# Performance work log

Measured on AMD Instinct MI355X. Metric: run time of the kernel, lower is better.

The kernel has to match this reference:

```python
import jax, jax.numpy as jnp
import numpy as np

B, N, C = 8, 4096, 1024
H, D = 16, 64
FF = 4096
EPS_ATTN = 1e-6
EPS_LN = 1e-5


def layer_norm(x, g, b, eps=EPS_LN):
    mu = jnp.mean(x, axis=-1, keepdims=True)
    var = jnp.mean(jnp.square(x - mu), axis=-1, keepdims=True)
    return (x - mu) * jax.lax.rsqrt(var + eps) * g + b


def phi(x):
    # elu(x) + 1
    return jnp.where(x > 0, x + 1.0, jnp.exp(x))


def setup_inputs() -> dict:
    key = jax.random.key(0)
    ks = jax.random.split(key, 8)
    src = jax.random.normal(ks[0], (B, N, C), dtype=jnp.float32)
    lengths = jax.random.randint(ks[1], (B,), int(0.75 * N), N + 1)
    src_key_padding_mask = jnp.arange(N)[None, :] >= lengths[:, None]
    s = 0.02
    qkv_w = jax.random.normal(ks[2], (3 * C, C), dtype=jnp.float32) * s
    qkv_b = jnp.zeros((3 * C,), jnp.float32)
    out_w = jax.random.normal(ks[3], (C, C), dtype=jnp.float32) * s
    out_b = jnp.zeros((C,), jnp.float32)
    w1 = jax.random.normal(ks[4], (FF, C), dtype=jnp.float32) * s
    b1 = jnp.zeros((FF,), jnp.float32)
    w2 = jax.random.normal(ks[5], (C, FF), dtype=jnp.float32) * s
    b2 = jnp.zeros((C,), jnp.float32)
    ln1_g = jnp.ones((C,), jnp.float32)
    ln1_b = jnp.zeros((C,), jnp.float32)
    ln2_g = jnp.ones((C,), jnp.float32)
    ln2_b = jnp.zeros((C,), jnp.float32)
    return dict(src=src, src_key_padding_mask=src_key_padding_mask,
                qkv_w=qkv_w, qkv_b=qkv_b, out_w=out_w, out_b=out_b,
                w1=w1, b1=b1, w2=w2, b2=b2,
                ln1_g=ln1_g, ln1_b=ln1_b, ln2_g=ln2_g, ln2_b=ln2_b)


def linear_attention(x, mask, qkv_w, qkv_b, out_w, out_b):
    b, n, c = x.shape
    qkv = (x @ qkv_w.T + qkv_b).reshape(b, n, 3, H, D)
    qkv = jnp.transpose(qkv, (2, 0, 3, 1, 4))  # [3,B,H,N,D]
    q, k, v = qkv[0], qkv[1], qkv[2]
    qf, kf = phi(q), phi(k)
    valid = (~mask).astype(kf.dtype)[:, None, :, None]  # [B,1,N,1]
    kf = kf * valid
    v = v * valid
    kv = jnp.einsum('bhnd,bhne->bhde', kf, v)          # [B,H,D,D]
    z = kf.sum(axis=2)                                  # [B,H,D]
    y_num = jnp.einsum('bhnd,bhde->bhne', qf, kv)       # [B,H,N,D]
    y_den = jnp.maximum(jnp.einsum('bhnd,bhd->bhn', qf, z), EPS_ATTN)
    y = y_num / y_den[..., None]
    y = jnp.transpose(y, (0, 2, 1, 3)).reshape(b, n, c)
    return y @ out_w.T + out_b


def reference(src, src_key_padding_mask, qkv_w, qkv_b, out_w, out_b,
              w1, b1, w2, b2, ln1_g, ln1_b, ln2_g, ln2_b):
    # pre-norm: attention block
    attn_out = linear_attention(layer_norm(src, ln1_g, ln1_b), src_key_padding_mask,
                                qkv_w, qkv_b, out_w, out_b)
    x = src + attn_out
    # pre-norm: FFN block (exact gelu, matching torch F.gelu default)
    h = jax.nn.gelu(layer_norm(x, ln2_g, ln2_b) @ w1.T + b1, approximate=False)
    return x + (h @ w2.T + b2)
```

## Files before the change

### kernel.cpp

```cpp
#include <hip/hip_runtime.h>
#include <cmath>
#include <cstdint>

#define MTOK 32768
#define CDIM 1024
#define SEQ  4096
#define NHEAD 16
#define HDIM 64
#define FFDIM 4096

typedef __attribute__((ext_vector_type(8))) short short8;
typedef __attribute__((ext_vector_type(4))) float f32x4;

static __device__ __forceinline__ float b2f(unsigned short u){
  union { unsigned int i; float f; } c; c.i = ((unsigned int)u)<<16; return c.f;
}
static __device__ __forceinline__ unsigned short f2b(float f){
  union { float f; unsigned int i; } c; c.f = f;
  return (unsigned short)((c.i + 0x7fffu + ((c.i>>16)&1u)) >> 16);
}
static __device__ __forceinline__ void async16(const void* g, void* l){
  __builtin_amdgcn_global_load_lds((const __attribute__((address_space(1))) void*)g,
                                   (__attribute__((address_space(3))) void*)l, 16, 0, 0);
}

__global__ void detect_mask_kernel(const unsigned int* __restrict__ m, int* __restrict__ flag){
  __shared__ int any;
  if(threadIdx.x==0) any=0;
  __syncthreads();
  int loc=0;
  for(int i=threadIdx.x;i<8192;i+=256) if(m[i]>1u) loc=1;
  if(loc) atomicOr(&any,1);
  __syncthreads();
  if(threadIdx.x==0) *flag=any;
}
__global__ void decode_mask_kernel(const void* __restrict__ m, const int* __restrict__ flag,
                                   float* __restrict__ validf){
  int i = blockIdx.x*256 + threadIdx.x;
  int pad = (*flag) ? (int)((const unsigned char*)m)[i] : ((const int*)m)[i];
  validf[i] = pad ? 0.f : 1.f;
}

__global__ void cast_bf16_kernel(const float* __restrict__ x, unsigned short* __restrict__ y, int n){
  int i = (blockIdx.x*256 + threadIdx.x)*4;
  if(i>=n) return;
  float4 v = *(const float4*)(x+i);
  ushort4 o; o.x=f2b(v.x); o.y=f2b(v.y); o.z=f2b(v.z); o.w=f2b(v.w);
  *(ushort4*)(y+i)=o;
}

__global__ __launch_bounds__(256) void ln_kernel(const float* __restrict__ x,
    const float* __restrict__ g, const float* __restrict__ bt, unsigned short* __restrict__ out){
  int row = blockIdx.x, t = threadIdx.x;
  const float* xr = x + (size_t)row*CDIM;
  float4 v = *(const float4*)(xr + t*4);
  float s1 = v.x+v.y+v.z+v.w;
  float s2 = v.x*v.x+v.y*v.y+v.z*v.z+v.w*v.w;
  #pragma unroll
  for(int off=32; off>0; off>>=1){ s1+=__shfl_down(s1,off); s2+=__shfl_down(s2,off); }
  __shared__ float a1[4], a2[4];
  __shared__ float mu_s, rs_s;
  if((t&63)==0){ a1[t>>6]=s1; a2[t>>6]=s2; }
  __syncthreads();
  if(t==0){
    float u1=a1[0]+a1[1]+a1[2]+a1[3], u2=a2[0]+a2[1]+a2[2]+a2[3];
    float mu=u1*(1.f/CDIM);
    mu_s=mu; rs_s=rsqrtf(u2*(1.f/CDIM)-mu*mu+1e-5f);
  }
  __syncthreads();
  float mu=mu_s, rs=rs_s;
  float4 gg=*(const float4*)(g+t*4), bb=*(const float4*)(bt+t*4);
  ushort4 o;
  o.x=f2b((v.x-mu)*rs*gg.x+bb.x);
  o.y=f2b((v.y-mu)*rs*gg.y+bb.y);
  o.z=f2b((v.z-mu)*rs*gg.z+bb.z);
  o.w=f2b((v.w-mu)*rs*gg.w+bb.w);
  *(ushort4*)(out+(size_t)row*CDIM+t*4)=o;
}

template<int MODE>
__global__ __launch_bounds__(256,2) void gemm_bt(
    const unsigned short* __restrict__ A, const unsigned short* __restrict__ Bw,
    const float* __restrict__ bias, const float* __restrict__ extra,
    float* __restrict__ Cf, unsigned short* __restrict__ Cb,
    int M, int N, int K)
{
  __shared__ __align__(16) unsigned short As[128*64];
  __shared__ __align__(16) unsigned short Bs[128*64];
  const int tid = threadIdx.x;
  const int wave = tid>>6, lane = tid&63;
  const int wm = wave>>1, wn = wave&1;
  const int f   = blockIdx.y * gridDim.x + blockIdx.x;
  const int xcd = f & 7, kk = f >> 3;
  const int nx  = kk % gridDim.x;
  const int ny  = (kk / gridDim.x) * 8 + xcd;
  const int m0 = ny*128, n0 = nx*128;
  const int lrow = lane>>3;
  const int gcol = (((lane&7) ^ lrow))*8;

  f32x4 acc[4][4];
  #pragma unroll
  for(int i=0;i<4;i++)
    #pragma unroll
    for(int j=0;j<4;j++) acc[i][j]=(f32x4)(0.f);

  const int ar = wm*64 + (lane&15);
  const int br = wn*64 + (lane&15);
  const int kc = lane>>4;
  const int xorv = lane&7;

  for(int kt=0; kt<K; kt+=64){
    #pragma unroll
    for(int it=0; it<4; it++){
      int wo = wave*4+it;
      int r  = wo*8 + lrow;
      async16(A  + (size_t)(m0+r)*K + kt + gcol, (void*)&As[wo*512]);
      async16(Bw + (size_t)(n0+r)*K + kt + gcol, (void*)&Bs[wo*512]);
    }
    __syncthreads();
    #pragma unroll
    for(int ks=0; ks<2; ks++){
      const int ch = ((ks*4 + kc) ^ xorv)*8;
      short8 a[4], b[4];
      #pragma unroll
      for(int i=0;i<4;i++){
        a[i]=*(const short8*)&As[(ar+i*16)*64 + ch];
        b[i]=*(const short8*)&Bs[(br+i*16)*64 + ch];
      }
      #pragma unroll
      for(int i=0;i<4;i++)
        #pragma unroll
        for(int j=0;j<4;j++)
          acc[i][j]=__builtin_amdgcn_mfma_f32_16x16x32_bf16(a[i],b[j],acc[i][j],0,0,0);
    }
    __syncthreads();
  }
  const int rbase = m0 + wm*64 + (lane>>4)*4;
  const int cbase = n0 + wn*64 + (lane&15);
  #pragma unroll
  for(int mi=0;mi<4;mi++){
    #pragma unroll
    for(int i=0;i<4;i++){
      int m = rbase + mi*16 + i;
      #pragma unroll
      for(int ni=0;ni<4;ni++){
        int n = cbase + ni*16;
        float v = acc[mi][ni][i] + bias[n];
        if(MODE==0){
          float valid = extra[m];
          int part = n>>10;
          float p = (v>0.f)? (v+1.f) : __expf(v);
          float r = (part==0)? p : (part==1? p*valid : v*valid);
          Cb[(size_t)m*N + n] = f2b(r);
        } else if(MODE==1){
          size_t off=(size_t)m*N+n;
          Cf[off] = v + extra[off];
        } else if(MODE==2){
          float gl = 0.5f*v*(1.f+erff(v*0.70710678118654752f));
          Cb[(size_t)m*N+n] = f2b(gl);
        } else {
          size_t off=(size_t)m*N+n;
          Cf[off] += v;
        }
      }
    }
  }
}

__global__ __launch_bounds__(256) void kvz_partial_kernel(
    const unsigned short* __restrict__ qkv, float* __restrict__ kvp, float* __restrict__ zp)
{
  const int chunk = blockIdx.x;
  const int bh = blockIdx.y;
  const int b = bh>>4, h = bh&15;
  const int t = threadIdx.x;
  __shared__ float kfs[16][64];
  __shared__ float vs[16][64];
  float acc[4][4]={{0}}; float zacc[4]={0};
  const int td=t&15, te=t>>4;
  const int d0=td*4, e0=te*4;
  const int lr=t>>4, lc=(t&15)*4;
  for(int s=0;s<16;s++){
    size_t m  = (size_t)(b*SEQ + chunk*256 + s*16 + lr);
    size_t rb = m*3072 + (size_t)h*64;
    ushort4 k4 = *(const ushort4*)(qkv + rb + 1024 + lc);
    ushort4 v4 = *(const ushort4*)(qkv + rb + 2048 + lc);
    __syncthreads();
    kfs[lr][lc]=b2f(k4.x); kfs[lr][lc+1]=b2f(k4.y); kfs[lr][lc+2]=b2f(k4.z); kfs[lr][lc+3]=b2f(k4.w);
    vs [lr][lc]=b2f(v4.x); vs [lr][lc+1]=b2f(v4.y); vs [lr][lc+2]=b2f(v4.z); vs [lr][lc+3]=b2f(v4.w);
    __syncthreads();
    #pragma unroll
    for(int n=0;n<16;n++){
      float4 kq=*(const float4*)&kfs[n][d0];
      float4 vv=*(const float4*)&vs[n][e0];
      float kqa[4]={kq.x,kq.y,kq.z,kq.w};
      float vva[4]={vv.x,vv.y,vv.z,vv.w};
      #pragma unroll
      for(int i=0;i<4;i++)
        #pragma unroll
        for(int j=0;j<4;j++) acc[i][j]+=kqa[i]*vva[j];
      if(te==0){ zacc[0]+=kq.x; zacc[1]+=kq.y; zacc[2]+=kq.z; zacc[3]+=kq.w; }
    }
  }
  const int pidx = bh*16 + chunk;
  float* kvd = kvp + (size_t)pidx*4096;
  #pragma unroll
  for(int i=0;i<4;i++){
    float4 o={acc[i][0],acc[i][1],acc[i][2],acc[i][3]};
    *(float4*)(kvd + (d0+i)*64 + e0)=o;
  }
  if(te==0){
    float4 o={zacc[0],zacc[1],zacc[2],zacc[3]};
    *(float4*)(zp + (size_t)pidx*64 + d0)=o;
  }
}

__global__ void kvz_reduce_kernel(const float* __restrict__ kvp, const float* __restrict__ zp,
                                  float* __restrict__ kv, float* __restrict__ z){
  int bh = blockIdx.x, t = threadIdx.x;
  for(int j=t; j<4096; j+=256){
    float s=0;
    for(int c=0;c<16;c++) s += kvp[((size_t)bh*16+c)*4096 + j];
    kv[(size_t)bh*4096 + j] = s;
  }
  if(t<64){
    float s=0;
    for(int c=0;c<16;c++) s += zp[((size_t)bh*16+c)*64 + t];
    z[bh*64+t]=s;
  }
}

__global__ __launch_bounds__(256) void y_kernel(
    const unsigned short* __restrict__ qkv, const float* __restrict__ kv,
    const float* __restrict__ z, unsigned short* __restrict__ ybuf)
{
  const int nch = blockIdx.x;
  const int bh  = blockIdx.y;
  const int b = bh>>4, h = bh&15;
  const int t = threadIdx.x;
  __shared__ float kvs[64][64];
  __shared__ float qfs[64][68];
  __shared__ float zs[64];
  for(int j=t*4; j<4096; j+=1024){
    float4 vv=*(const float4*)(kv+(size_t)bh*4096+j);
    ((float*)kvs)[j]=vv.x; ((float*)kvs)[j+1]=vv.y; ((float*)kvs)[j+2]=vv.z; ((float*)kvs)[j+3]=vv.w;
  }
  if(t<64) zs[t]=z[bh*64+t];
  for(int s=0;s<4;s++){
    int row=s*16+(t>>4), col=(t&15)*4;
    size_t m=(size_t)(b*SEQ+nch*64+row);
    ushort4 q4=*(const ushort4*)(qkv+m*3072+(size_t)h*64+col);
    qfs[row][col]=b2f(q4.x); qfs[row][col+1]=b2f(q4.y); qfs[row][col+2]=b2f(q4.z); qfs[row][col+3]=b2f(q4.w);
  }
  __syncthreads();
  const int tn=t>>4, te=t&15;
  const int nr0=tn*4, e0=te*4;
  float acc[4][4]={{0}}; float den[4]={0};
  #pragma unroll 4
  for(int d=0;d<64;d++){
    float4 kv4=*(const float4*)&kvs[d][e0];
    float zd=zs[d];
    #pragma unroll
    for(int i=0;i<4;i++){
      float q=qfs[nr0+i][d];
      acc[i][0]+=q*kv4.x; acc[i][1]+=q*kv4.y; acc[i][2]+=q*kv4.z; acc[i][3]+=q*kv4.w;
      den[i]+=q*zd;
    }
  }
  #pragma unroll
  for(int i=0;i<4;i++){
    float inv=1.f/fmaxf(den[i],1e-6f);
    ushort4 o;
    o.x=f2b(acc[i][0]*inv); o.y=f2b(acc[i][1]*inv); o.z=f2b(acc[i][2]*inv); o.w=f2b(acc[i][3]*inv);
    size_t m=(size_t)(b*SEQ+nch*64+nr0+i);
    *(ushort4*)(ybuf+m*1024+(size_t)h*64+e0)=o;
  }
}

extern "C" void kernel_launch(void* const* d_in, const int* in_sizes, int n_in,
                              void* d_out, int out_size, void* d_ws, size_t ws_size,
                              hipStream_t stream)
{
  const float* src   = (const float*)d_in[0];
  const void*  mask  = d_in[1];
  const float* qkv_w = (const float*)d_in[2];
  const float* qkv_b = (const float*)d_in[3];
  const float* out_w = (const float*)d_in[4];
  const float* out_b = (const float*)d_in[5];
  const float* w1    = (const float*)d_in[6];
  const float* b1    = (const float*)d_in[7];
  const float* w2    = (const float*)d_in[8];
  const float* b2    = (const float*)d_in[9];
  const float* ln1g  = (const float*)d_in[10];
  const float* ln1b  = (const float*)d_in[11];
  const float* ln2g  = (const float*)d_in[12];
  const float* ln2b  = (const float*)d_in[13];
  float* out = (float*)d_out;
  char* ws = (char*)d_ws;

  size_t o = 0;
  int* flag = (int*)(ws);                         o += 256;
  float* validf = (float*)(ws+o);                 o += (size_t)MTOK*4;
  unsigned short* wqb = (unsigned short*)(ws+o);  o += (size_t)3072*1024*2;
  unsigned short* wob = (unsigned short*)(ws+o);  o += (size_t)1024*1024*2;
  unsigned short* w1b = (unsigned short*)(ws+o);  o += (size_t)4096*1024*2;
  unsigned short* w2b = (unsigned short*)(ws+o);  o += (size_t)1024*4096*2;
  unsigned short* bufA = (unsigned short*)(ws+o); o += (size_t)MTOK*1024*2;
  char* R = ws+o;                                 o += (size_t)MTOK*4096*2;
  unsigned short* qkvbuf = (unsigned short*)R;
  float* kvp = (float*)(R + (size_t)MTOK*3072*2);
  float* zp  = (float*)(R + (size_t)MTOK*3072*2 + (size_t)2048*4096*4);
  unsigned short* hbuf = (unsigned short*)R;
  float* kv = (float*)(ws+o);                     o += (size_t)128*4096*4;
  float* zv = (float*)(ws+o);                     o += (size_t)128*64*4;

  detect_mask_kernel<<<1,256,0,stream>>>((const unsigned int*)mask, flag);
  decode_mask_kernel<<<MTOK/256,256,0,stream>>>(mask, flag, validf);
  cast_bf16_kernel<<<3072,256,0,stream>>>(qkv_w, wqb, 3072*1024);
  cast_bf16_kernel<<<1024,256,0,stream>>>(out_w, wob, 1024*1024);
  cast_bf16_kernel<<<4096,256,0,stream>>>(w1,  w1b, 4096*1024);
  cast_bf16_kernel<<<8192,256,0,stream>>>(w2,  w2b, 1024*4096);

  ln_kernel<<<MTOK,256,0,stream>>>(src, ln1g, ln1b, bufA);
  gemm_bt<0><<<dim3(3072/128, MTOK/128),256,0,stream>>>(bufA, wqb, qkv_b, validf, nullptr, qkvbuf, MTOK,3072,1024);
  kvz_partial_kernel<<<dim3(16,128),256,0,stream>>>(qkvbuf, kvp, zp);
  kvz_reduce_kernel<<<128,256,0,stream>>>(kvp, zp, kv, zv);
  y_kernel<<<dim3(64,128),256,0,stream>>>(qkvbuf, kv, zv, bufA);
  gemm_bt<1><<<dim3(1024/128, MTOK/128),256,0,stream>>>(bufA, wob, out_b, src, out, nullptr, MTOK,1024,1024);
  ln_kernel<<<MTOK,256,0,stream>>>(out, ln2g, ln2b, bufA);
  gemm_bt<2><<<dim3(4096/128, MTOK/128),256,0,stream>>>(bufA, w1b, b1, nullptr, nullptr, hbuf, MTOK,4096,1024);
  gemm_bt<3><<<dim3(1024/128, MTOK/128),256,0,stream>>>(hbuf, w2b, b2, nullptr, out, nullptr, MTOK,1024,4096);
}
```

Before: 1.471 ms.

## Rewrite GEMM as 256x256 tile, 8-wave, double-buffered pipelined kernel

The bf16 GEMM moves from 128x128 tiles with 4 waves and a single LDS buffer to 256x256 tiles with 8 waves and double-buffered LDS. Global-to-LDS async loads for the next K-step are issued between four quadrant MFMA phases, with explicit vmcnt/lgkmcnt waits, barriers and s_setprio raising priority around the MFMA bursts. The aim is to overlap memory traffic with matrix math and raise arithmetic intensity per tile. In exchange it uses more LDS and registers per block, launches fewer blocks (the out-projection and FFN2 GEMMs get only 512 blocks), and its correctness rests on hand-tuned wait counts.

```diff
diff --git a/kernel.cpp b/kernel.cpp
--- a/kernel.cpp
+++ b/kernel.cpp
@@ -79,88 +79,148 @@
 }
 
 template<int MODE>
-__global__ __launch_bounds__(256,2) void gemm_bt(
+__global__ __launch_bounds__(512,2) void gemm_bt(
     const unsigned short* __restrict__ A, const unsigned short* __restrict__ Bw,
     const float* __restrict__ bias, const float* __restrict__ extra,
     float* __restrict__ Cf, unsigned short* __restrict__ Cb,
     int M, int N, int K)
 {
-  __shared__ __align__(16) unsigned short As[128*64];
-  __shared__ __align__(16) unsigned short Bs[128*64];
-  const int tid = threadIdx.x;
-  const int wave = tid>>6, lane = tid&63;
-  const int wm = wave>>1, wn = wave&1;
-  const int f   = blockIdx.y * gridDim.x + blockIdx.x;
+  __shared__ __align__(16) unsigned short As[2*2*128*64];
+  __shared__ __align__(16) unsigned short Bs[2*2*128*64];
+  const int tid  = threadIdx.x;
+  const int lane = tid & 63, wave = tid >> 6;
+  const int wm = wave >> 2, wn = wave & 3;
+  const int gx  = gridDim.x;
+  const int f   = blockIdx.y * gx + blockIdx.x;
   const int xcd = f & 7, kk = f >> 3;
-  const int nx  = kk % gridDim.x;
-  const int ny  = (kk / gridDim.x) * 8 + xcd;
-  const int m0 = ny*128, n0 = nx*128;
-  const int lrow = lane>>3;
-  const int gcol = (((lane&7) ^ lrow))*8;
-
-  f32x4 acc[4][4];
-  #pragma unroll
-  for(int i=0;i<4;i++)
+  const int nx  = kk % gx;
+  const int ny  = (kk / gx) * 8 + xcd;
+  const int m0 = ny*256, n0 = nx*256;
+  const int r8  = lane >> 3;
+  const int gch = ((lane & 7) ^ r8) * 8;
+  const int l15 = lane & 15;
+  const int kc  = lane >> 4, x7 = lane & 7;
+  const int ch0 = ( kc      ^ x7) * 8;
+  const int ch1 = ((kc + 4) ^ x7) * 8;
+  const int NT  = K >> 6;
+
+  f32x4 acc[2][2][4][2];
+  #pragma unroll
+  for(int a0=0;a0<2;a0++)
     #pragma unroll
-    for(int j=0;j<4;j++) acc[i][j]=(f32x4)(0.f);
-
-  const int ar = wm*64 + (lane&15);
-  const int br = wn*64 + (lane&15);
-  const int kc = lane>>4;
-  const int xorv = lane&7;
-
-  for(int kt=0; kt<K; kt+=64){
+    for(int a1=0;a1<2;a1++)
+      #pragma unroll
+      for(int a2=0;a2<4;a2++)
+        #pragma unroll
+        for(int a3=0;a3<2;a3++) acc[a0][a1][a2][a3]=(f32x4)(0.f);
+
+  auto stageA = [&](int h, int bb, int kcol){
+    const unsigned short* g = A + (size_t)(m0 + h*128 + wave*8 + r8)*K + kcol + gch;
+    unsigned short* l = &As[((bb*2 + h)*128 + wave*8)*64];
+    async16(g, l);
+    async16(g + (size_t)64*K, l + 64*64);
+  };
+  auto stageB = [&](int h, int bb, int kcol){
+    const unsigned short* g = Bw + (size_t)(n0 + h*128 + wave*8 + r8)*K + kcol + gch;
+    unsigned short* l = &Bs[((bb*2 + h)*128 + wave*8)*64];
+    async16(g, l);
+    async16(g + (size_t)64*K, l + 64*64);
+  };
+
+  #define READ_A(H,BB) { const unsigned short* Ab=&As[((BB)*2+(H))*128*64];         \
+    _Pragma("unroll") for(int fi=0;fi<4;fi++){ int ro=(wm*64+fi*16+l15)*64;          \
+      af[fi][0]=*(const short8*)&Ab[ro+ch0];                                         \
+      af[fi][1]=*(const short8*)&Ab[ro+ch1]; } }
+  #define READ_B(H,BB,DST) { const unsigned short* Bb=&Bs[((BB)*2+(H))*128*64];      \
+    _Pragma("unroll") for(int ni=0;ni<2;ni++){ int ro=(wn*32+ni*16+l15)*64;          \
+      DST[ni][0]=*(const short8*)&Bb[ro+ch0];                                        \
+      DST[ni][1]=*(const short8*)&Bb[ro+ch1]; } }
+  #define QUAD(MQ,NQ,BV) {                                                           \
+    _Pragma("unroll") for(int fi=0;fi<4;fi++)                                        \
+      _Pragma("unroll") for(int ni=0;ni<2;ni++){                                     \
+        acc[MQ][NQ][fi][ni]=__builtin_amdgcn_mfma_f32_16x16x32_bf16(                 \
+            af[fi][0],BV[ni][0],acc[MQ][NQ][fi][ni],0,0,0);                          \
+        acc[MQ][NQ][fi][ni]=__builtin_amdgcn_mfma_f32_16x16x32_bf16(                 \
+            af[fi][1],BV[ni][1],acc[MQ][NQ][fi][ni],0,0,0); } }
+
+  stageA(0,0,0); stageA(1,0,0); stageB(0,0,0); stageB(1,0,0);
+  if(NT>1){
+    stageA(0,1,64); stageB(0,1,64);
+    asm volatile("s_waitcnt vmcnt(4)" ::: "memory");
+  } else {
+    asm volatile("s_waitcnt vmcnt(0)" ::: "memory");
+  }
+  __builtin_amdgcn_s_barrier();
+
+  for(int t=0; t<NT; ++t){
+    const int bi = t & 1, bo = (t+1) & 1;
+    const int k1 = (t+1) << 6, k2 = (t+2) << 6;
+    short8 af[4][2], b0v[2][2], b1v[2][2];
+
+    READ_A(0,bi); READ_B(0,bi,b0v);
+    if(t+1<NT) stageA(1,bo,k1);
+    __builtin_amdgcn_s_barrier();
+    asm volatile("s_waitcnt lgkmcnt(0)" ::: "memory");
+    __builtin_amdgcn_s_setprio(1); QUAD(0,0,b0v); __builtin_amdgcn_s_setprio(0);
+    __builtin_amdgcn_s_barrier();
+
+    READ_B(1,bi,b1v);
+    if(t+1<NT) stageB(1,bo,k1);
+    __builtin_amdgcn_s_barrier();
+    asm volatile("s_waitcnt lgkmcnt(0)" ::: "memory");
+    __builtin_amdgcn_s_setprio(1); QUAD(0,1,b1v); __builtin_amdgcn_s_setprio(0);
+    __builtin_amdgcn_s_barrier();
+
+    READ_A(1,bi);
+    if(t+2<NT) stageA(0,bi,k2);
+    __builtin_amdgcn_s_barrier();
+    asm volatile("s_waitcnt lgkmcnt(0)" ::: "memory");
+    __builtin_amdgcn_s_setprio(1); QUAD(1,0,b0v); __builtin_amdgcn_s_setprio(0);
+    __builtin_amdgcn_s_barrier();
+
+    if(t+2<NT) stageB(0,bi,k2);
+    __builtin_amdgcn_s_barrier();
+    asm volatile("s_waitcnt lgkmcnt(0)" ::: "memory");
+    __builtin_amdgcn_s_setprio(1); QUAD(1,1,b1v); __builtin_amdgcn_s_setprio(0);
+    if(t+2<NT){ asm volatile("s_waitcnt vmcnt(4)" ::: "memory"); }
+    else      { asm volatile("s_waitcnt vmcnt(0)" ::: "memory"); }
+    __builtin_amdgcn_s_barrier();
+  }
+  #undef READ_A
+  #undef READ_B
+  #undef QUAD
+
+  const int rb0 = (lane>>4)*4;
+  #pragma unroll
+  for(int mq=0;mq<2;mq++){
     #pragma unroll
-    for(int it=0; it<4; it++){
-      int wo = wave*4+it;
-      int r  = wo*8 + lrow;
-      async16(A  + (size_t)(m0+r)*K + kt + gcol, (void*)&As[wo*512]);
-      async16(Bw + (size_t)(n0+r)*K + kt + gcol, (void*)&Bs[wo*512]);
-    }
-    __syncthreads();
-    #pragma unroll
-    for(int ks=0; ks<2; ks++){
-      const int ch = ((ks*4 + kc) ^ xorv)*8;
-      short8 a[4], b[4];
+    for(int fi=0;fi<4;fi++){
       #pragma unroll
       for(int i=0;i<4;i++){
-        a[i]=*(const short8*)&As[(ar+i*16)*64 + ch];
-        b[i]=*(const short8*)&Bs[(br+i*16)*64 + ch];
-      }
-      #pragma unroll
-      for(int i=0;i<4;i++)
+        int m = m0 + mq*128 + wm*64 + fi*16 + rb0 + i;
+        float valid = (MODE==0) ? extra[m] : 0.f;
         #pragma unroll
-        for(int j=0;j<4;j++)
-          acc[i][j]=__builtin_amdgcn_mfma_f32_16x16x32_bf16(a[i],b[j],acc[i][j],0,0,0);
-    }
-    __syncthreads();
-  }
-  const int rbase = m0 + wm*64 + (lane>>4)*4;
-  const int cbase = n0 + wn*64 + (lane&15);
-  #pragma unroll
-  for(int mi=0;mi<4;mi++){
-    #pragma unroll
-    for(int i=0;i<4;i++){
-      int m = rbase + mi*16 + i;
-      #pragma unroll
-      for(int ni=0;ni<4;ni++){
-        int n = cbase + ni*16;
-        float v = acc[mi][ni][i] + bias[n];
-        if(MODE==0){
-          float valid = extra[m];
-          int part = n>>10;
-          float p = (v>0.f)? (v+1.f) : __expf(v);
-          float r = (part==0)? p : (part==1? p*valid : v*valid);
-          Cb[(size_t)m*N + n] = f2b(r);
-        } else if(MODE==1){
-          size_t off=(size_t)m*N+n;
-          Cf[off] = v + extra[off];
-        } else if(MODE==2){
-          float gl = 0.5f*v*(1.f+erff(v*0.70710678118654752f));
-          Cb[(size_t)m*N+n] = f2b(gl);
-        } else {
-          size_t off=(size_t)m*N+n;
-          Cf[off] += v;
+        for(int nq=0;nq<2;nq++){
+          #pragma unroll
+          for(int ni=0;ni<2;ni++){
+            int n = n0 + nq*128 + wn*32 + ni*16 + l15;
+            float v = acc[mq][nq][fi][ni][i] + bias[n];
+            if(MODE==0){
+              int part = n>>10;
+              float p = (v>0.f)? (v+1.f) : __expf(v);
+              float r = (part==0)? p : (part==1? p*valid : v*valid);
+              Cb[(size_t)m*N + n] = f2b(r);
+            } else if(MODE==1){
+              size_t off=(size_t)m*N+n;
+              Cf[off] = v + extra[off];
+            } else if(MODE==2){
+              float gl = 0.5f*v*(1.f+erff(v*0.70710678118654752f));
+              Cb[(size_t)m*N+n] = f2b(gl);
+            } else {
+              size_t off=(size_t)m*N+n;
+              Cf[off] += v;
+            }
+          }
         }
       }
     }
@@ -322,12 +382,12 @@
   cast_bf16_kernel<<<8192,256,0,stream>>>(w2,  w2b, 1024*4096);
 
   ln_kernel<<<MTOK,256,0,stream>>>(src, ln1g, ln1b, bufA);
-  gemm_bt<0><<<dim3(3072/128, MTOK/128),256,0,stream>>>(bufA, wqb, qkv_b, validf, nullptr, qkvbuf, MTOK,3072,1024);
+  gemm_bt<0><<<dim3(3072/256, MTOK/256),512,0,stream>>>(bufA, wqb, qkv_b, validf, nullptr, qkvbuf, MTOK,3072,1024);
   kvz_partial_kernel<<<dim3(16,128),256,0,stream>>>(qkvbuf, kvp, zp);
   kvz_reduce_kernel<<<128,256,0,stream>>>(kvp, zp, kv, zv);
   y_kernel<<<dim3(64,128),256,0,stream>>>(qkvbuf, kv, zv, bufA);
-  gemm_bt<1><<<dim3(1024/128, MTOK/128),256,0,stream>>>(bufA, wob, out_b, src, out, nullptr, MTOK,1024,1024);
+  gemm_bt<1><<<dim3(1024/256, MTOK/256),512,0,stream>>>(bufA, wob, out_b, src, out, nullptr, MTOK,1024,1024);
   ln_kernel<<<MTOK,256,0,stream>>>(out, ln2g, ln2b, bufA);
-  gemm_bt<2><<<dim3(4096/128, MTOK/128),256,0,stream>>>(bufA, w1b, b1, nullptr, nullptr, hbuf, MTOK,4096,1024);
-  gemm_bt<3><<<dim3(1024/128, MTOK/128),256,0,stream>>>(hbuf, w2b, b2, nullptr, out, nullptr, MTOK,1024,4096);
-}
+  gemm_bt<2><<<dim3(4096/256, MTOK/256),512,0,stream>>>(bufA, w1b, b1, nullptr, nullptr, hbuf, MTOK,4096,1024);
+  gemm_bt<3><<<dim3(1024/256, MTOK/256),512,0,stream>>>(hbuf, w2b, b2, nullptr, out, nullptr, MTOK,1024,4096);
+}
```

Result: slower. 1.561 ms (+6.1%).
